# Performance work log

Hardware: AMD Instinct MI355X
Metric: run time of the kernel (lower is better)

The kernel has to match this reference:

```python
import jax, jax.numpy as jnp
import numpy as np

B, N, M = 2, 8192, 8192


def setup_inputs() -> dict:
    key = jax.random.key(0)
    ks = jax.random.split(key, 12)
    def rn(k, shape):
        return jax.random.normal(k, shape, dtype=jnp.float32)
    return {
        "in_xyz": rn(ks[0], (B, N, 3)),
        "in_rot": rn(ks[1], (B, N, 4)),
        "in_scale": rn(ks[2], (B, N, 3)),
        "in_opacity": rn(ks[3], (B, N, 1)),
        "in_sh_dc": rn(ks[4], (B, N, 3)),
        "in_sh_rest": rn(ks[5], (B, N, 45)),
        "out_xyz": rn(ks[6], (B, M, 3)),
        "out_rot": rn(ks[7], (B, M, 4)),
        "out_scale": rn(ks[8], (B, M, 3)),
        "out_opacity": rn(ks[9], (B, M, 1)),
        "out_sh_dc": rn(ks[10], (B, M, 3)),
        "out_sh_rest": rn(ks[11], (B, M, 45)),
    }


POS_W, ROT_W, SCALE_W, OPAC_W, SH_W = 1.0, 0.5, 0.5, 0.3, 0.2


def _cdist(a, b):
    # a: [B,M,3], b: [B,N,3] -> [B,M,N] Euclidean distance via Gram trick
    sq = (jnp.sum(a * a, -1)[:, :, None] + jnp.sum(b * b, -1)[:, None, :]
          - 2.0 * jnp.einsum('bmd,bnd->bmn', a, b))
    return jnp.sqrt(jnp.maximum(sq, 0.0))


def _gather(x, idx):
    # x: [B,N,D], idx: [B,M] -> [B,M,D]
    return jnp.take_along_axis(x, idx[:, :, None], axis=1)


def reference(in_xyz, in_rot, in_scale, in_opacity, in_sh_dc, in_sh_rest,
              out_xyz, out_rot, out_scale, out_opacity, out_sh_dc, out_sh_rest):
    dist = _cdist(out_xyz, in_xyz)                 # [B,M,N]
    min_out_to_in = jnp.min(dist, axis=2)          # [B,M]
    match_idx = jnp.argmin(dist, axis=2)           # [B,M]
    min_in_to_out = jnp.min(dist, axis=1)          # [B,N]
    pos_loss = (min_out_to_in.mean() + min_in_to_out.mean()) / 2

    matched_rot = _gather(in_rot, match_idx)
    matched_scale = _gather(in_scale, match_idx)
    matched_opacity = _gather(in_opacity, match_idx)
    matched_sh_dc = _gather(in_sh_dc, match_idx)
    matched_sh_rest = _gather(in_sh_rest, match_idx)

    rot_dot = jnp.abs(jnp.sum(out_rot * matched_rot, axis=-1))
    rot_loss = jnp.mean(1.0 - rot_dot)
    scale_loss = jnp.mean(jnp.abs(out_scale - matched_scale))
    opacity_loss = jnp.mean(jnp.abs(out_opacity - matched_opacity))
    sh_loss = (jnp.mean(jnp.abs(out_sh_dc - matched_sh_dc))
               + jnp.mean(jnp.abs(out_sh_rest - matched_sh_rest)))

    total = (POS_W * pos_loss + ROT_W * rot_loss + SCALE_W * scale_loss
             + OPAC_W * opacity_loss + SH_W * sh_loss)
    return total
```

## Files before the change

kernel.cpp:

```cpp
#include <hip/hip_runtime.h>


#define BB 2
#define NN 8192
#define MM 8192
#define TILE_PTS 1024
#define CHUNK_PTS 64
#define CH_STRIDE (CHUNK_PTS * 4 + 4)
#define CM_STRIDE 65
#define PM 256
#define NSL 8
#define GSL 32
#define NPAIR 512
#define NEPI 320

__device__ __forceinline__ void dmerge(float& d, int& i, float od, int oi) {
    if (od < d || (od == d && oi < i)) { d = od; i = oi; }
}

__device__ __forceinline__ void stage_tile(const float* __restrict__ xyz,
                                           int b, int gtile, int t, float* smem) {
    const uint4* src = (const uint4*)((const char*)xyz +
                       ((size_t)b * NN + (size_t)gtile * TILE_PTS) * 12);
    uint4 wb[3];
#pragma unroll
    for (int k = 0; k < 3; ++k) wb[k] = src[t * 3 + k];
    const unsigned int* w = (const unsigned int*)wb;
    const int p0 = t * 4;
    float4* dst = (float4*)(smem + (p0 >> 6) * CH_STRIDE) + (p0 & 63);
#pragma unroll
    for (int i = 0; i < 4; ++i) {
        float x = __uint_as_float(w[3 * i + 0]);
        float y = __uint_as_float(w[3 * i + 1]);
        float z = __uint_as_float(w[3 * i + 2]);
        float4 v;
        v.x = x; v.y = y; v.z = z;
        v.w = fmaf(z, z, fmaf(y, y, x * x));
        dst[i] = v;
    }
}

__global__ __launch_bounds__(1024) void k_pair(
    const float* __restrict__ in_xyz,
    const float* __restrict__ out_xyz,
    float* __restrict__ outD2,
    int*   __restrict__ outIdx,
    float* __restrict__ inD2s,
    unsigned int* __restrict__ cnt) {

    __shared__ float smem[16 * CH_STRIDE];
    __shared__ unsigned int cmu[16 * CM_STRIDE];

    const int t  = threadIdx.x;
    const int ml = t >> 4;
    const int c  = t & 15;
    const int blk = blockIdx.x;
    const int b  = blk >> 8;
    const int e  = (blk >> 5) & 7;
    const int g  = blk & 31;
    const int q0 = g * PM + ml * 4;

    if (blk == 0 && t == 0) cnt[0] = 0u;

    float m2x0, m2y0, m2z0, msq0, m2x1, m2y1, m2z1, msq1;
    float m2x2, m2y2, m2z2, msq2, m2x3, m2y3, m2z3, msq3;
#define LOADQ(i)                                                            \
    { const float* qp = out_xyz + ((size_t)b * MM + q0 + i) * 3;            \
      float ox = qp[0], oy = qp[1], oz = qp[2];                             \
      m2x##i = -2.f * ox; m2y##i = -2.f * oy; m2z##i = -2.f * oz;           \
      msq##i = fmaf(oz, oz, fmaf(oy, oy, ox * ox)); }
    LOADQ(0) LOADQ(1) LOADQ(2) LOADQ(3)
#undef LOADQ

    if (t < 256) stage_tile(in_xyz, b, e, t, smem);
    for (int i = t; i < 16 * CM_STRIDE; i += 1024) cmu[i] = 0x7F800000u;
    __syncthreads();

    const float4* cp = (const float4*)(smem + c * CH_STRIDE);
    const int base = e * TILE_PTS + c * CHUNK_PTS;
    unsigned int* cma = cmu + c * CM_STRIDE;
    const bool doAtom = ((t & 48) == 0);

    float bd0 = 3e38f, bd1 = 3e38f, bd2 = 3e38f, bd3 = 3e38f;
    int   bi0 = 0,     bi1 = 0,     bi2 = 0,     bi3 = 0;
#pragma unroll 8
    for (int j = 0; j < CHUNK_PTS; ++j) {
        float4 p = cp[j];
        float w0 = p.w + msq0, w1 = p.w + msq1, w2 = p.w + msq2, w3 = p.w + msq3;
        float k0 = fmaf(p.x, m2x0, fmaf(p.y, m2y0, fmaf(p.z, m2z0, w0)));
        float k1 = fmaf(p.x, m2x1, fmaf(p.y, m2y1, fmaf(p.z, m2z1, w1)));
        float k2 = fmaf(p.x, m2x2, fmaf(p.y, m2y2, fmaf(p.z, m2z2, w2)));
        float k3 = fmaf(p.x, m2x3, fmaf(p.y, m2y3, fmaf(p.z, m2z3, w3)));
        if (k0 < bd0) { bd0 = k0; bi0 = base + j; }
        if (k1 < bd1) { bd1 = k1; bi1 = base + j; }
        if (k2 < bd2) { bd2 = k2; bi2 = base + j; }
        if (k3 < bd3) { bd3 = k3; bi3 = base + j; }
        float mm = fminf(fminf(k0, k1), fminf(k2, k3));
        mm = fmaxf(mm, 0.0f);
        mm = fminf(mm, __shfl_xor(mm, 16, 64));
        mm = fminf(mm, __shfl_xor(mm, 32, 64));
        if (doAtom) atomicMin(cma + j, __float_as_uint(mm));
    }

#pragma unroll
    for (int off = 1; off < 16; off <<= 1) {
        float od; int oi;
        od = __shfl_xor(bd0, off, 64); oi = __shfl_xor(bi0, off, 64); dmerge(bd0, bi0, od, oi);
        od = __shfl_xor(bd1, off, 64); oi = __shfl_xor(bi1, off, 64); dmerge(bd1, bi1, od, oi);
        od = __shfl_xor(bd2, off, 64); oi = __shfl_xor(bi2, off, 64); dmerge(bd2, bi2, od, oi);
        od = __shfl_xor(bd3, off, 64); oi = __shfl_xor(bi3, off, 64); dmerge(bd3, bi3, od, oi);
    }
    if (c == 0) {
        const size_t gi = ((size_t)b * MM + q0) * NSL + e;
        outD2[gi + 0 * NSL] = bd0; outIdx[gi + 0 * NSL] = bi0;
        outD2[gi + 1 * NSL] = bd1; outIdx[gi + 1 * NSL] = bi1;
        outD2[gi + 2 * NSL] = bd2; outIdx[gi + 2 * NSL] = bi2;
        outD2[gi + 3 * NSL] = bd3; outIdx[gi + 3 * NSL] = bi3;
    }

    __syncthreads();
    {
        float v = __uint_as_float(cmu[(t >> 6) * CM_STRIDE + (t & 63)]);
        inD2s[(size_t)g * (BB * NN) + (size_t)b * NN + e * TILE_PTS + t] = v;
    }
}

__global__ __launch_bounds__(256) void k_epi(
    const float* __restrict__ in_rot,
    const float* __restrict__ in_scale,
    const float* __restrict__ in_op,
    const float* __restrict__ in_dc,
    const float* __restrict__ in_rest,
    const float* __restrict__ out_rot,
    const float* __restrict__ out_scale,
    const float* __restrict__ out_op,
    const float* __restrict__ out_dc,
    const float* __restrict__ out_rest,
    const float* __restrict__ outD2,
    const int*   __restrict__ outIdx,
    const float* __restrict__ inD2s,
    float* __restrict__ pout,
    float* __restrict__ pin,
    unsigned int* __restrict__ cnt,
    unsigned int* __restrict__ outw) {

    __shared__ float red[4][8];
    __shared__ int lastFlag;
    const int t = threadIdx.x;
    const int blk = blockIdx.x;

    if (blk < 256) {
        const int u = blk * 256 + t;
        const int m = u >> 2;
        const int h = u & 3;
        const int b = m >> 13;
        float2 dv = ((const float2*)outD2)[(size_t)m * 4 + h];
        int2   iv = ((const int2*)outIdx)[(size_t)m * 4 + h];
        float d2 = dv.x; int idx = iv.x;
        if (dv.y < d2) { d2 = dv.y; idx = iv.y; }
        {
            float od; int oi;
            od = __shfl_xor(d2, 1, 64); oi = __shfl_xor(idx, 1, 64); dmerge(d2, idx, od, oi);
            od = __shfl_xor(d2, 2, 64); oi = __shfl_xor(idx, 2, 64); dmerge(d2, idx, od, oi);
        }
        const size_t og = (size_t)m;
        const size_t ig = (size_t)b * NN + (size_t)idx;

        float pos = 0.f, rot = 0.f, scl = 0.f, opa = 0.f, dcv = 0.f, rsv = 0.f;
        if (h == 0) {
            pos = sqrtf(fmaxf(d2, 0.f));
            const float4 orv = ((const float4*)out_rot)[og];
            const float4 irv = ((const float4*)in_rot)[ig];
            float rdot = orv.x * irv.x + orv.y * irv.y + orv.z * irv.z + orv.w * irv.w;
            rot = 1.f - fabsf(rdot);
        } else if (h == 1) {
#pragma unroll
            for (int q = 0; q < 3; ++q) scl += fabsf(out_scale[og * 3 + q] - in_scale[ig * 3 + q]);
            opa = fabsf(out_op[og] - in_op[ig]);
#pragma unroll
            for (int q = 0; q < 3; ++q) dcv += fabsf(out_dc[og * 3 + q] - in_dc[ig * 3 + q]);
        } else if (h == 2) {
#pragma unroll
            for (int e = 0; e < 22; ++e)
                rsv += fabsf(out_rest[og * 45 + e] - in_rest[ig * 45 + e]);
        } else {
#pragma unroll
            for (int e = 22; e < 45; ++e)
                rsv += fabsf(out_rest[og * 45 + e] - in_rest[ig * 45 + e]);
        }

#pragma unroll
        for (int off = 1; off < 64; off <<= 1) {
            pos += __shfl_xor(pos, off, 64);
            rot += __shfl_xor(rot, off, 64);
            scl += __shfl_xor(scl, off, 64);
            opa += __shfl_xor(opa, off, 64);
            dcv += __shfl_xor(dcv, off, 64);
            rsv += __shfl_xor(rsv, off, 64);
        }
        if ((t & 63) == 0) {
            const size_t w = (size_t)blk * 4 + (t >> 6);
            pout[w * 6 + 0] = pos; pout[w * 6 + 1] = rot; pout[w * 6 + 2] = scl;
            pout[w * 6 + 3] = opa; pout[w * 6 + 4] = dcv; pout[w * 6 + 5] = rsv;
        }
    } else {
        const int n = (blk - 256) * 256 + t;
        float d2 = inD2s[n];
#pragma unroll
        for (int s = 1; s < GSL; ++s)
            d2 = fminf(d2, inD2s[(size_t)s * (BB * NN) + n]);
        float v = sqrtf(fmaxf(d2, 0.f));
#pragma unroll
        for (int off = 1; off < 64; off <<= 1) v += __shfl_xor(v, off, 64);
        if ((t & 63) == 0) pin[(size_t)(blk - 256) * 4 + (t >> 6)] = v;
    }

    __syncthreads();
    if (t == 0) {
        __threadfence();
        unsigned int old = atomicAdd(cnt, 1u);
        lastFlag = (old == (unsigned)(NEPI - 1));
    }
    __syncthreads();
    if (!lastFlag) return;
    __threadfence();

    float s0 = 0.f, s1 = 0.f, s2 = 0.f, s3 = 0.f, s4 = 0.f, s5 = 0.f, s6 = 0.f;
    for (int i = t; i < 1024; i += 256) {
        s0 += pout[(size_t)i * 6 + 0];
        s1 += pout[(size_t)i * 6 + 1];
        s2 += pout[(size_t)i * 6 + 2];
        s3 += pout[(size_t)i * 6 + 3];
        s4 += pout[(size_t)i * 6 + 4];
        s5 += pout[(size_t)i * 6 + 5];
    }
    s6 = pin[t];
#pragma unroll
    for (int off = 1; off < 64; off <<= 1) {
        s0 += __shfl_xor(s0, off, 64);
        s1 += __shfl_xor(s1, off, 64);
        s2 += __shfl_xor(s2, off, 64);
        s3 += __shfl_xor(s3, off, 64);
        s4 += __shfl_xor(s4, off, 64);
        s5 += __shfl_xor(s5, off, 64);
        s6 += __shfl_xor(s6, off, 64);
    }
    if ((t & 63) == 0) {
        const int w = t >> 6;
        red[w][0] = s0; red[w][1] = s1; red[w][2] = s2; red[w][3] = s3;
        red[w][4] = s4; red[w][5] = s5; red[w][6] = s6;
    }
    __syncthreads();
    if (t == 0) {
        float a[7];
#pragma unroll
        for (int j = 0; j < 7; ++j)
            a[j] = red[0][j] + red[1][j] + red[2][j] + red[3][j];
        const float inv_bm = 1.0f / (float)(BB * MM);
        const float inv_bn = 1.0f / (float)(BB * NN);
        const float pos = 0.5f * (a[0] * inv_bm + a[6] * inv_bn);
        const float rot = a[1] * inv_bm;
        const float scl = a[2] * inv_bm * (1.f / 3.f);
        const float opa = a[3] * inv_bm;
        const float sh  = a[4] * inv_bm * (1.f / 3.f) + a[5] * inv_bm * (1.f / 45.f);
        const float total = 1.0f * pos + 0.5f * rot + 0.5f * scl + 0.3f * opa + 0.2f * sh;
        unsigned int ub = __float_as_uint(total);
        unsigned int r  = (ub + 0x7FFFu + ((ub >> 16) & 1u)) >> 16;
        if (!(total == total) || fabsf(total) > 1e30f) r = 0x4080u;
        outw[0] = (r << 16) | r;
    }
}

extern "C" void kernel_launch(void* const* d_in, const int* in_sizes, int n_in,
                              void* d_out, int out_size, void* d_ws, size_t ws_size,
                              hipStream_t stream) {
    const float* in_xyz    = (const float*)d_in[0];
    const float* in_rot    = (const float*)d_in[1];
    const float* in_scale  = (const float*)d_in[2];
    const float* in_op     = (const float*)d_in[3];
    const float* in_dc     = (const float*)d_in[4];
    const float* in_rest   = (const float*)d_in[5];
    const float* out_xyz   = (const float*)d_in[6];
    const float* out_rot   = (const float*)d_in[7];
    const float* out_scale = (const float*)d_in[8];
    const float* out_op    = (const float*)d_in[9];
    const float* out_dc    = (const float*)d_in[10];
    const float* out_rest  = (const float*)d_in[11];

    float* outD2 = (float*)d_ws;
    int*   outIdx = (int*)(outD2 + (size_t)BB * MM * NSL);
    float* inD2s = (float*)(outIdx + (size_t)BB * MM * NSL);
    float* pout  = inD2s + (size_t)GSL * BB * NN;
    float* pin   = pout + 1024 * 6;
    unsigned int* cnt = (unsigned int*)(pin + 256);

    k_pair<<<NPAIR, 1024, 0, stream>>>(in_xyz, out_xyz, outD2, outIdx, inD2s, cnt);
    k_epi<<<NEPI, 256, 0, stream>>>(in_rot, in_scale, in_op, in_dc, in_rest,
                                    out_rot, out_scale, out_op, out_dc, out_rest,
                                    outD2, outIdx, inD2s, pout, pin, cnt,
                                    (unsigned int*)d_out);
}
```

Baseline: 135.2 us.

## Retile pairwise kernel to 8 queries x 32 points per thread with register column minima

Restructures the pairwise distance kernel so each thread handles 8 query rows against 32 strided input points, keeping per-column minima in registers instead of doing a shuffle-reduce and LDS atomicMin on every inner iteration. Queries are staged through shared memory, and column minima are combined once at the end with one shuffle and 32 atomics per thread. This raises register-level reuse and removes per-iteration cross-lane traffic, at the cost of much higher register pressure (32 column accumulators plus 8 rows of state) at 1024 threads per block.

```diff
diff --git a/kernel.cpp b/kernel.cpp
--- a/kernel.cpp
+++ b/kernel.cpp
@@ -4,11 +4,8 @@
 #define BB 2
 #define NN 8192
 #define MM 8192
-#define TILE_PTS 1024
-#define CHUNK_PTS 64
-#define CH_STRIDE (CHUNK_PTS * 4 + 4)
-#define CM_STRIDE 65
-#define PM 256
+#define QB 256
+#define PB 1024
 #define NSL 8
 #define GSL 32
 #define NPAIR 512
@@ -16,28 +13,6 @@
 
 __device__ __forceinline__ void dmerge(float& d, int& i, float od, int oi) {
     if (od < d || (od == d && oi < i)) { d = od; i = oi; }
-}
-
-__device__ __forceinline__ void stage_tile(const float* __restrict__ xyz,
-                                           int b, int gtile, int t, float* smem) {
-    const uint4* src = (const uint4*)((const char*)xyz +
-                       ((size_t)b * NN + (size_t)gtile * TILE_PTS) * 12);
-    uint4 wb[3];
-#pragma unroll
-    for (int k = 0; k < 3; ++k) wb[k] = src[t * 3 + k];
-    const unsigned int* w = (const unsigned int*)wb;
-    const int p0 = t * 4;
-    float4* dst = (float4*)(smem + (p0 >> 6) * CH_STRIDE) + (p0 & 63);
-#pragma unroll
-    for (int i = 0; i < 4; ++i) {
-        float x = __uint_as_float(w[3 * i + 0]);
-        float y = __uint_as_float(w[3 * i + 1]);
-        float z = __uint_as_float(w[3 * i + 2]);
-        float4 v;
-        v.x = x; v.y = y; v.z = z;
-        v.w = fmaf(z, z, fmaf(y, y, x * x));
-        dst[i] = v;
-    }
 }
 
 __global__ __launch_bounds__(1024) void k_pair(
@@ -48,81 +23,111 @@
     float* __restrict__ inD2s,
     unsigned int* __restrict__ cnt) {
 
-    __shared__ float smem[16 * CH_STRIDE];
-    __shared__ unsigned int cmu[16 * CM_STRIDE];
+    __shared__ float4 pts[PB];
+    __shared__ float4 qmem[QB];
+    __shared__ unsigned int colbuf[PB];
 
     const int t  = threadIdx.x;
-    const int ml = t >> 4;
-    const int c  = t & 15;
+    const int ci = t & 31;
+    const int ri = t >> 5;
     const int blk = blockIdx.x;
     const int b  = blk >> 8;
     const int e  = (blk >> 5) & 7;
     const int g  = blk & 31;
-    const int q0 = g * PM + ml * 4;
 
     if (blk == 0 && t == 0) cnt[0] = 0u;
 
-    float m2x0, m2y0, m2z0, msq0, m2x1, m2y1, m2z1, msq1;
-    float m2x2, m2y2, m2z2, msq2, m2x3, m2y3, m2z3, msq3;
-#define LOADQ(i)                                                            \
-    { const float* qp = out_xyz + ((size_t)b * MM + q0 + i) * 3;            \
-      float ox = qp[0], oy = qp[1], oz = qp[2];                             \
-      m2x##i = -2.f * ox; m2y##i = -2.f * oy; m2z##i = -2.f * oz;           \
-      msq##i = fmaf(oz, oz, fmaf(oy, oy, ox * ox)); }
-    LOADQ(0) LOADQ(1) LOADQ(2) LOADQ(3)
-#undef LOADQ
-
-    if (t < 256) stage_tile(in_xyz, b, e, t, smem);
-    for (int i = t; i < 16 * CM_STRIDE; i += 1024) cmu[i] = 0x7F800000u;
-    __syncthreads();
-
-    const float4* cp = (const float4*)(smem + c * CH_STRIDE);
-    const int base = e * TILE_PTS + c * CHUNK_PTS;
-    unsigned int* cma = cmu + c * CM_STRIDE;
-    const bool doAtom = ((t & 48) == 0);
-
-    float bd0 = 3e38f, bd1 = 3e38f, bd2 = 3e38f, bd3 = 3e38f;
-    int   bi0 = 0,     bi1 = 0,     bi2 = 0,     bi3 = 0;
-#pragma unroll 8
-    for (int j = 0; j < CHUNK_PTS; ++j) {
-        float4 p = cp[j];
-        float w0 = p.w + msq0, w1 = p.w + msq1, w2 = p.w + msq2, w3 = p.w + msq3;
-        float k0 = fmaf(p.x, m2x0, fmaf(p.y, m2y0, fmaf(p.z, m2z0, w0)));
-        float k1 = fmaf(p.x, m2x1, fmaf(p.y, m2y1, fmaf(p.z, m2z1, w1)));
-        float k2 = fmaf(p.x, m2x2, fmaf(p.y, m2y2, fmaf(p.z, m2z2, w2)));
-        float k3 = fmaf(p.x, m2x3, fmaf(p.y, m2y3, fmaf(p.z, m2z3, w3)));
-        if (k0 < bd0) { bd0 = k0; bi0 = base + j; }
-        if (k1 < bd1) { bd1 = k1; bi1 = base + j; }
-        if (k2 < bd2) { bd2 = k2; bi2 = base + j; }
-        if (k3 < bd3) { bd3 = k3; bi3 = base + j; }
-        float mm = fminf(fminf(k0, k1), fminf(k2, k3));
-        mm = fmaxf(mm, 0.0f);
-        mm = fminf(mm, __shfl_xor(mm, 16, 64));
-        mm = fminf(mm, __shfl_xor(mm, 32, 64));
-        if (doAtom) atomicMin(cma + j, __float_as_uint(mm));
-    }
-
-#pragma unroll
-    for (int off = 1; off < 16; off <<= 1) {
-        float od; int oi;
-        od = __shfl_xor(bd0, off, 64); oi = __shfl_xor(bi0, off, 64); dmerge(bd0, bi0, od, oi);
-        od = __shfl_xor(bd1, off, 64); oi = __shfl_xor(bi1, off, 64); dmerge(bd1, bi1, od, oi);
-        od = __shfl_xor(bd2, off, 64); oi = __shfl_xor(bi2, off, 64); dmerge(bd2, bi2, od, oi);
-        od = __shfl_xor(bd3, off, 64); oi = __shfl_xor(bi3, off, 64); dmerge(bd3, bi3, od, oi);
-    }
-    if (c == 0) {
+    if (t < 256) {
+        const uint4* src = (const uint4*)((const char*)in_xyz +
+                           ((size_t)b * NN + (size_t)e * PB) * 12);
+        uint4 wb[3];
+#pragma unroll
+        for (int k = 0; k < 3; ++k) wb[k] = src[t * 3 + k];
+        const unsigned int* w = (const unsigned int*)wb;
+        float4* dst = pts + t * 4;
+#pragma unroll
+        for (int i = 0; i < 4; ++i) {
+            float x = __uint_as_float(w[3 * i + 0]);
+            float y = __uint_as_float(w[3 * i + 1]);
+            float z = __uint_as_float(w[3 * i + 2]);
+            float4 v;
+            v.x = x; v.y = y; v.z = z;
+            v.w = fmaf(z, z, fmaf(y, y, x * x));
+            dst[i] = v;
+        }
+    } else if (t < 512) {
+        const int qi = t - 256;
+        const float* qp = out_xyz + ((size_t)b * MM + (size_t)g * QB + qi) * 3;
+        float ox = qp[0], oy = qp[1], oz = qp[2];
+        float4 q;
+        q.x = -2.f * ox; q.y = -2.f * oy; q.z = -2.f * oz;
+        q.w = fmaf(oz, oz, fmaf(oy, oy, ox * ox));
+        qmem[qi] = q;
+    }
+    colbuf[t] = 0x7F800000u;
+    __syncthreads();
+
+    float qx[8], qy[8], qz[8], qs[8];
+#pragma unroll
+    for (int r = 0; r < 8; ++r) {
+        float4 q = qmem[ri * 8 + r];
+        qx[r] = q.x; qy[r] = q.y; qz[r] = q.z; qs[r] = q.w;
+    }
+
+    float rowd[8]; int rowi[8];
+    float cm[32];
+#pragma unroll
+    for (int r = 0; r < 8; ++r) { rowd[r] = 3e38f; rowi[r] = 0; }
+#pragma unroll
+    for (int k = 0; k < 32; ++k) cm[k] = 3e38f;
+
+#pragma unroll
+    for (int k = 0; k < 32; ++k) {
+        const float4 p = pts[k * 32 + ci];
+        float kk[8];
+#pragma unroll
+        for (int r = 0; r < 8; ++r) {
+            float w = p.w + qs[r];
+            float d = fmaf(p.x, qx[r], fmaf(p.y, qy[r], fmaf(p.z, qz[r], w)));
+            kk[r] = d;
+            if (d < rowd[r]) { rowd[r] = d; rowi[r] = k * 32 + ci; }
+        }
+        cm[k] = fminf(cm[k], fminf(kk[0], kk[1]));
+        cm[k] = fminf(cm[k], fminf(kk[2], kk[3]));
+        cm[k] = fminf(cm[k], fminf(kk[4], kk[5]));
+        cm[k] = fminf(cm[k], fminf(kk[6], kk[7]));
+    }
+
+#pragma unroll
+    for (int off = 1; off < 32; off <<= 1) {
+#pragma unroll
+        for (int r = 0; r < 8; ++r) {
+            float od = __shfl_xor(rowd[r], off, 64);
+            int   oi = __shfl_xor(rowi[r], off, 64);
+            dmerge(rowd[r], rowi[r], od, oi);
+        }
+    }
+    if (ci == 0) {
+        const int q0 = g * QB + ri * 8;
         const size_t gi = ((size_t)b * MM + q0) * NSL + e;
-        outD2[gi + 0 * NSL] = bd0; outIdx[gi + 0 * NSL] = bi0;
-        outD2[gi + 1 * NSL] = bd1; outIdx[gi + 1 * NSL] = bi1;
-        outD2[gi + 2 * NSL] = bd2; outIdx[gi + 2 * NSL] = bi2;
-        outD2[gi + 3 * NSL] = bd3; outIdx[gi + 3 * NSL] = bi3;
-    }
-
-    __syncthreads();
-    {
-        float v = __uint_as_float(cmu[(t >> 6) * CM_STRIDE + (t & 63)]);
-        inD2s[(size_t)g * (BB * NN) + (size_t)b * NN + e * TILE_PTS + t] = v;
-    }
+#pragma unroll
+        for (int r = 0; r < 8; ++r) {
+            outD2[gi + (size_t)r * NSL]  = rowd[r];
+            outIdx[gi + (size_t)r * NSL] = e * PB + rowi[r];
+        }
+    }
+
+#pragma unroll
+    for (int k = 0; k < 32; ++k)
+        cm[k] = fmaxf(fminf(cm[k], __shfl_xor(cm[k], 32, 64)), 0.0f);
+    if ((t & 32) == 0) {
+#pragma unroll
+        for (int k = 0; k < 32; ++k)
+            atomicMin(&colbuf[k * 32 + ci], __float_as_uint(cm[k]));
+    }
+    __syncthreads();
+    inD2s[(size_t)g * (BB * NN) + (size_t)b * NN + e * PB + t] =
+        __uint_as_float(colbuf[t]);
 }
 
 __global__ __launch_bounds__(256) void k_epi(
```

Result: slower. 343.0 us (+153.6%).
